# Performance work log

Measured on AMD Instinct MI355X. Metric: run time of the kernel, lower is better.

The kernel has to match this reference:

```python
import jax, jax.numpy as jnp
import numpy as np
import math

N_NODES, CHANNELS, N_ELEM, N_FEAT = 4096, 128, 10, 128
LS_IN = [0, 1, 2]          # input irreps per channel: 0e+1o+2e -> dim 9
L_OUT = [0, 1]             # keep_irrep_out = {0e, 1o}
L12_MAX = 3                # cap on intermediate coupling
SLICES = {0: (0, 1), 1: (1, 4), 2: (4, 9)}
PATHS1 = [l for l in L_OUT if l in LS_IN]
PATHS2 = [(l1, l2, lo) for l1 in LS_IN for l2 in LS_IN for lo in L_OUT if abs(l1 - l2) <= lo <= l1 + l2]
T12_KEYS = [(l1, l2, l12) for l1 in LS_IN for l2 in LS_IN for l12 in range(abs(l1 - l2), min(l1 + l2, L12_MAX) + 1)]
PATHS3 = [(k, l3, lo) for k in T12_KEYS for l3 in LS_IN for lo in L_OUT if abs(k[2] - l3) <= lo <= k[2] + l3]

def _su2_cg(j1, m1, j2, m2, j3, m3):
    if m3 != m1 + m2:
        return 0.0
    f = math.factorial
    vmin = max(-j1 + j2 + m3, -j1 + m1, 0)
    vmax = min(j2 + j3 + m1, j3 - j1 + j2, j3 + m3)
    C = math.sqrt((2 * j3 + 1) * f(j3 + j1 - j2) * f(j3 - j1 + j2) * f(j1 + j2 - j3) * f(j3 + m3) * f(j3 - m3)
                  / (f(j1 + j2 + j3 + 1) * f(j1 - m1) * f(j1 + m1) * f(j2 - m2) * f(j2 + m2)))
    S = 0.0
    for v in range(vmin, vmax + 1):
        S += (-1) ** (v + j2 + m2) * f(j2 + j3 + m1 - v) * f(j1 - m1 + v) / (
            f(v) * f(j3 - j1 + j2 - v) * f(j3 + m3 - v) * f(v + j1 - j2 - m3))
    return C * S

def _c2r(l):
    # change of basis real -> complex spherical harmonics (e3nn convention)
    q = np.zeros((2 * l + 1, 2 * l + 1), dtype=np.complex128)
    for m in range(-l, 0):
        q[l + m, l + abs(m)] = 1.0 / math.sqrt(2)
        q[l + m, l - abs(m)] = -1j / math.sqrt(2)
    q[l, l] = 1.0
    for m in range(1, l + 1):
        q[l + m, l + abs(m)] = (-1) ** m / math.sqrt(2)
        q[l + m, l - abs(m)] = 1j * (-1) ** m / math.sqrt(2)
    return (-1j) ** l * q

_CG = {}
def real_cg(l1, l2, l3):
    key = (l1, l2, l3)
    if key not in _CG:
        Cc = np.zeros((2 * l1 + 1, 2 * l2 + 1, 2 * l3 + 1), dtype=np.complex128)
        for i, m1 in enumerate(range(-l1, l1 + 1)):
            for j, m2 in enumerate(range(-l2, l2 + 1)):
                for k, m3 in enumerate(range(-l3, l3 + 1)):
                    Cc[i, j, k] = _su2_cg(l1, m1, l2, m2, l3, m3)
        R = np.einsum('ij,kl,mn,ikn->jlm', _c2r(l1), _c2r(l2), np.conj(_c2r(l3).T), Cc)
        _CG[key] = np.real(R).astype(np.float32)
    return _CG[key]

def setup_inputs():
    key = jax.random.key(0)
    k = jax.random.split(key, 8)
    node_feats = jax.random.normal(k[0], (N_NODES, CHANNELS, 9), dtype=jnp.float32)
    species = jax.random.randint(k[1], (N_NODES,), 0, N_ELEM)
    w1 = jax.random.normal(k[2], (N_ELEM, len(PATHS1), CHANNELS), dtype=jnp.float32) / math.sqrt(len(PATHS1))
    w2 = jax.random.normal(k[3], (N_ELEM, len(PATHS2), CHANNELS), dtype=jnp.float32) / math.sqrt(len(PATHS2))
    w3 = jax.random.normal(k[4], (N_ELEM, len(PATHS3), CHANNELS), dtype=jnp.float32) / math.sqrt(len(PATHS3))
    lin_w0 = jax.random.normal(k[5], (CHANNELS, N_FEAT), dtype=jnp.float32)
    lin_w1 = jax.random.normal(k[6], (CHANNELS, N_FEAT), dtype=jnp.float32)
    return {"node_feats": node_feats, "w1": w1, "w2": w2, "w3": w3,
            "lin_w0": lin_w0, "lin_w1": lin_w1, "species": species}

def reference(node_feats, w1, w2, w3, lin_w0, lin_w1, species):
    n, c = node_feats.shape[:2]
    attrs = jax.nn.one_hot(species, N_ELEM, dtype=node_feats.dtype)
    A = {l: node_feats[..., SLICES[l][0]:SLICES[l][1]] for l in LS_IN}
    # element-dependent path weights per node
    w1n = jnp.einsum('ne,epc->npc', attrs, w1)
    w2n = jnp.einsum('ne,epc->npc', attrs, w2)
    w3n = jnp.einsum('ne,epc->npc', attrs, w3)
    B = {lo: jnp.zeros((n, c, 2 * lo + 1), node_feats.dtype) for lo in L_OUT}
    # correlation order 1
    for p, lo in enumerate(PATHS1):
        B[lo] = B[lo] + w1n[:, p, :, None] * A[lo]
    for p, (l1, l2, lo) in enumerate(PATHS2):
        cg = jnp.asarray(real_cg(l1, l2, lo))
        t = jnp.einsum('ijk,nci,ncj->nck', cg, A[l1], A[l2])
        B[lo] = B[lo] + w2n[:, p, :, None] * t
    T12 = {}
    for kk in T12_KEYS:
        l1, l2, l12 = kk
        T12[kk] = jnp.einsum('ijk,nci,ncj->nck', jnp.asarray(real_cg(l1, l2, l12)), A[l1], A[l2])
    for p, (kk, l3, lo) in enumerate(PATHS3):
        cg = jnp.asarray(real_cg(kk[2], l3, lo))
        t = jnp.einsum('ijk,nci,ncj->nck', cg, T12[kk], A[l3])
        B[lo] = B[lo] + w3n[:, p, :, None] * t
    # equivariant Linear: mix channel axis into num_features per output irrep
    s = 1.0 / math.sqrt(c)
    out0 = jnp.einsum('ncm,cf->nfm', B[0], lin_w0) * s
    out1 = jnp.einsum('ncm,cf->nfm', B[1], lin_w1) * s
    return jnp.concatenate([out0, out1], axis=-1)  # [N, F, 1+3]
```

## Files before the change

### kernel.cpp

```cpp
#include <hip/hip_runtime.h>
#include <utility>


#define NN 4096
#define NC 128
#define NE 10

typedef float v2f __attribute__((ext_vector_type(2)));
typedef __bf16 bf16x8 __attribute__((ext_vector_type(8)));
typedef float f32x4 __attribute__((ext_vector_type(4)));

__device__ __forceinline__ v2f ld2(const float* p) {
  return *reinterpret_cast<const v2f*>(p);
}
__device__ __forceinline__ v2f cfma(float c, v2f x, v2f a) {
  v2f cc = {c, c};
  return __builtin_elementwise_fma(cc, x, a);
}
__device__ __forceinline__ v2f vfma(v2f w, v2f x, v2f a) {
  return __builtin_elementwise_fma(w, x, a);
}

__device__ __forceinline__ unsigned short f2bf(float x) {
  unsigned int u = __float_as_uint(x);
  unsigned int r = (u + 0x7FFFu + ((u >> 16) & 1u)) >> 16;
  return (unsigned short)r;
}
__device__ __forceinline__ float bf2f(unsigned short h) {
  return __uint_as_float(((unsigned int)h) << 16);
}

template<typename F, int... Is>
__device__ __forceinline__ void sfor_impl(F&& f, std::integer_sequence<int, Is...>) {
  (f(std::integral_constant<int, Is>{}), ...);
}
template<int N, typename F>
__device__ __forceinline__ void sfor(F&& f) {
  sfor_impl((F&&)f, std::make_integer_sequence<int, N>{});
}

constexpr int T_L1c[19]  = {0,0,0,1,1,1,1,1,1,1,2,2,2,2,2,2,2,2,3};
constexpr int T_L2c[19]  = {0,1,2,0,1,1,1,2,2,2,0,1,1,1,2,2,2,2,2};
constexpr int T_L3c[19]  = {0,1,2,1,0,1,2,1,2,3,2,1,2,3,0,1,2,3,1};
constexpr int T_OFFc[19] = {0,1,10,35,44,53,80,125,170,245,350,375,420,495,600,625,700,825,1000};
constexpr int AOFFc[3]   = {0,1,4};

constexpr int P2U_L1c[7]  = {0,0,1,1,1,2,2};
constexpr int P2U_L2c[7]  = {0,1,1,1,2,2,2};
constexpr int P2U_LOc[7]  = {0,1,0,1,1,0,1};
constexpr int P2U_TBLc[7] = {0,1,4,5,7,14,15};
constexpr int P2U_WAc[7]  = {0,1,3,4,5,7,8};
constexpr int P2U_WBc[7]  = {-1,2,-1,-1,6,-1,-1};

constexpr int K_L1c[18]  = {0,0,0,1,1,1,1,1,1,1,2,2,2,2,2,2,2,2};
constexpr int K_L2c[18]  = {0,1,2,0,1,1,1,2,2,2,0,1,1,1,2,2,2,2};
constexpr int K_L12c[18] = {0,1,2,1,0,1,2,1,2,3,2,1,2,3,0,1,2,3};

constexpr int   TT_CANONc[18] = {0,1,2,1,4,5,6,7,8,9,2,7,8,9,14,15,16,17};
constexpr float TT_SGNc[18]   = {1,1,1,1,1,1,1,1,1,1,1,1,-1,1,1,1,1,1};
constexpr int CANONc[13] = {0,1,2,4,5,6,7,8,9,14,15,16,17};
constexpr int CONS2c[13] = {-1,3,10,-1,-1,-1,11,12,13,-1,-1,-1,-1};

constexpr int P3_STARTc[19] = {0,2,6,9,13,15,19,22,26,29,30,33,37,40,41,43,47,50,51};
constexpr int P3_L3c[51] = {
  0,1,  0,1,1,2,  1,2,2,  0,1,1,2,  0,1,  0,1,1,2,  1,2,2,  0,1,1,2,  1,2,2,
  2,  1,2,2,  0,1,1,2,  1,2,2,  2,  0,1,  0,1,1,2,  1,2,2,  2 };
constexpr int P3_LOc[51] = {
  0,1,  1,0,1,1,  1,0,1,  1,0,1,1,  0,1,  1,0,1,1,  1,0,1,  1,0,1,1,  1,0,1,
  1,  1,0,1,  1,0,1,1,  1,0,1,  1,  0,1,  1,0,1,1,  1,0,1,  1 };
constexpr int P3_TBLc[51] = {
  0,1,  3,4,5,7,  11,14,15,  3,4,5,7,  0,1,  3,4,5,7,  11,14,15,  3,4,5,7,
  11,14,15,  18,  11,14,15,  3,4,5,7,  11,14,15,  18,  0,1,  3,4,5,7,
  11,14,15,  18 };

constexpr double cfact(int n) { double r = 1.0; for (int i = 2; i <= n; ++i) r *= i; return r; }
constexpr double csqrt(double x) {
  if (x <= 0.0) return 0.0;
  double r = x > 1.0 ? x : 1.0;
  for (int i = 0; i < 64; ++i) r = 0.5 * (r + x / r);
  return r;
}
constexpr double su2cg(int j1, int m1, int j2, int m2, int j3, int m3) {
  if (m3 != m1 + m2) return 0.0;
  int vmin = -j1 + j2 + m3; if (-j1 + m1 > vmin) vmin = -j1 + m1; if (vmin < 0) vmin = 0;
  int vmax = j2 + j3 + m1; if (j3 - j1 + j2 < vmax) vmax = j3 - j1 + j2; if (j3 + m3 < vmax) vmax = j3 + m3;
  double C = csqrt((2.0 * j3 + 1.0)
                   * cfact(j3 + j1 - j2) * cfact(j3 - j1 + j2) * cfact(j1 + j2 - j3)
                   * cfact(j3 + m3) * cfact(j3 - m3)
                   / (cfact(j1 + j2 + j3 + 1) * cfact(j1 - m1) * cfact(j1 + m1)
                      * cfact(j2 - m2) * cfact(j2 + m2)));
  double S = 0.0;
  for (int v = vmin; v <= vmax; ++v) {
    double sgn = ((v + j2 + m2) & 1) ? -1.0 : 1.0;
    S += sgn * cfact(j2 + j3 + m1 - v) * cfact(j1 - m1 + v)
         / (cfact(v) * cfact(j3 - j1 + j2 - v) * cfact(j3 + m3 - v) * cfact(v + j1 - j2 - m3));
  }
  return C * S;
}

struct Cx { double re, im; };
constexpr Cx cxmul(Cx a, Cx b) { return Cx{a.re * b.re - a.im * b.im, a.re * b.im + a.im * b.re}; }
struct Row { int cnt; int col[2]; Cx v[2]; };

constexpr Row c2r_row(int l, int r) {
  Row out{0, {0, 0}, {{0, 0}, {0, 0}}};
  constexpr double is2 = 0.70710678118654752440;
  const int m = r - l;
  if (m < 0) {
    out.cnt = 2;
    out.col[0] = l - m; out.v[0] = Cx{is2, 0.0};
    out.col[1] = l + m; out.v[1] = Cx{0.0, -is2};
  } else if (m == 0) {
    out.cnt = 1; out.col[0] = l; out.v[0] = Cx{1.0, 0.0};
  } else {
    const double sgn = (m & 1) ? -1.0 : 1.0;
    out.cnt = 2;
    out.col[0] = l + m; out.v[0] = Cx{sgn * is2, 0.0};
    out.col[1] = l - m; out.v[1] = Cx{0.0, sgn * is2};
  }
  const int ph = l & 3;
  for (int a = 0; a < out.cnt; ++a) {
    Cx v = out.v[a];
    out.v[a] = (ph == 0) ? v
             : (ph == 1) ? Cx{v.im, -v.re}
             : (ph == 2) ? Cx{-v.re, -v.im}
                         : Cx{-v.im, v.re};
  }
  return out;
}

struct CGAll { float v[1105]; };
constexpr CGAll make_cg() {
  CGAll R{};
  for (int t = 0; t < 19; ++t) {
    const int l1 = T_L1c[t], l2 = T_L2c[t], l3 = T_L3c[t], off = T_OFFc[t];
    const int d1 = 2 * l1 + 1, d2 = 2 * l2 + 1, d3 = 2 * l3 + 1;
    double tmp[175] = {};
    for (int i = 0; i < d1; ++i) {
      const int m1 = i - l1;
      const Row r1 = c2r_row(l1, i);
      for (int k = 0; k < d2; ++k) {
        const int m2 = k - l2, m3 = m1 + m2;
        if (m3 < -l3 || m3 > l3) continue;
        const double cc = su2cg(l1, m1, l2, m2, l3, m3);
        if (cc == 0.0) continue;
        const Row r2 = c2r_row(l2, k);
        const Row r3 = c2r_row(l3, m3 + l3);
        for (int a = 0; a < r1.cnt; ++a)
          for (int b = 0; b < r2.cnt; ++b) {
            const Cx q12 = cxmul(r1.v[a], r2.v[b]);
            for (int cdx = 0; cdx < r3.cnt; ++cdx) {
              const double re = q12.re * r3.v[cdx].re + q12.im * r3.v[cdx].im;
              tmp[(r1.col[a] * d2 + r2.col[b]) * d3 + r3.col[cdx]] += re * cc;
            }
          }
      }
    }
    const int sz = d1 * d2 * d3;
    for (int e = 0; e < sz; ++e) R.v[off + e] = (float)tmp[e];
  }
  return R;
}
constexpr CGAll CG_ALL = make_cg();

constexpr bool check_cg_sym() {
  for (int t = 0; t < 18; ++t) {
    const int tc = TT_CANONc[t];
    if (tc == t) continue;
    const int l1 = K_L1c[t], l2 = K_L2c[t], l12 = K_L12c[t];
    const int d1 = 2*l1+1, d2 = 2*l2+1, d12 = 2*l12+1;
    for (int i = 0; i < d1; ++i)
      for (int j = 0; j < d2; ++j)
        for (int k = 0; k < d12; ++k) {
          float a = CG_ALL.v[T_OFFc[t]  + (i*d2 + j)*d12 + k];
          float b = TT_SGNc[t] * CG_ALL.v[T_OFFc[tc] + (j*d1 + i)*d12 + k];
          float d = a - b; if (d < 0) d = -d;
          if (d > 1e-5f) return false;
        }
  }
  return true;
}
static_assert(check_cg_sym(), "CG exchange symmetry violated");

__global__ __launch_bounds__(256) void epb_basis(
    const float* __restrict__ nf,
    const float* __restrict__ w1,
    const float* __restrict__ w2,
    const float* __restrict__ w3,
    const int*   __restrict__ species,
    unsigned int* __restrict__ AhiW,
    unsigned int* __restrict__ AloW)
{
  const int t  = threadIdx.x;
  const int nb = blockIdx.x * 4;
  const int nl = t >> 6;
  const int c0 = (t & 63) * 2;
  const int n  = nb + nl;
  const int s  = species[n];

  const float* ap = nf + ((size_t)n * NC + c0) * 9;
  v2f A[9];
  sfor<9>([&](auto I) { A[I.value] = v2f{ap[I.value], ap[I.value + 9]}; });

  const float* w1p = w1 + (size_t)s * 2  * NC + c0;
  const float* w2p = w2 + (size_t)s * 9  * NC + c0;
  const float* w3p = w3 + (size_t)s * 51 * NC + c0;

  v2f B[4];
  {
    const v2f wa = ld2(w1p), wb = ld2(w1p + NC);
    B[0] = wa * A[0];
    B[1] = wb * A[1];
    B[2] = wb * A[2];
    B[3] = wb * A[3];
  }

  sfor<7>([&](auto P) {
    constexpr int p  = P.value;
    constexpr int l1 = P2U_L1c[p], l2 = P2U_L2c[p], lo = P2U_LOc[p];
    constexpr int d1 = 2*l1+1, d2 = 2*l2+1, dl = 2*lo+1;
    constexpr int off = T_OFFc[P2U_TBLc[p]];
    v2f w = ld2(w2p + P2U_WAc[p] * NC);
    if constexpr (P2U_WBc[p] >= 0) w = w + ld2(w2p + P2U_WBc[p] * NC);
    sfor<dl>([&](auto Kk) {
      constexpr int k = Kk.value;
      v2f v = {0.f, 0.f};
      sfor<d1>([&](auto I) {
        sfor<d2>([&](auto J) {
          constexpr float cgc = CG_ALL.v[off + (I.value * d2 + J.value) * dl + k];
          if constexpr (cgc != 0.0f) {
            constexpr int ia = AOFFc[l1] + I.value, ja = AOFFc[l2] + J.value;
            constexpr int x = ia < ja ? ia : ja, y = ia < ja ? ja : ia;
            v = cfma(cgc, A[x] * A[y], v);
          }
        });
      });
      B[lo + k] = vfma(w, v, B[lo + k]);
    });
  });

  sfor<13>([&](auto CI) {
    constexpr int tk  = CANONc[CI.value];
    constexpr int l1  = K_L1c[tk], l2 = K_L2c[tk], l12 = K_L12c[tk];
    constexpr int d1  = 2*l1+1, d2 = 2*l2+1, d12 = 2*l12+1;
    constexpr int off = T_OFFc[tk];
    v2f tt[d12];
    sfor<d12>([&](auto Kk) {
      constexpr int k = Kk.value;
      v2f v = {0.f, 0.f};
      sfor<d1>([&](auto I) {
        sfor<d2>([&](auto J) {
          constexpr float cgc = CG_ALL.v[off + (I.value * d2 + J.value) * d12 + k];
          if constexpr (cgc != 0.0f) {
            constexpr int ia = AOFFc[l1] + I.value, ja = AOFFc[l2] + J.value;
            constexpr int x = ia < ja ? ia : ja, y = ia < ja ? ja : ia;
            v = cfma(cgc, A[x] * A[y], v);
          }
        });
      });
      tt[k] = v;
    });

    auto consume = [&](auto TK, auto SG) {
      constexpr int tkey = TK.value;
      constexpr float sgn = (float)SG.value;
      constexpr int pcnt = P3_STARTc[tkey + 1] - P3_STARTc[tkey];
      sfor<pcnt>([&](auto PP) {
        constexpr int p  = P3_STARTc[tkey] + PP.value;
        constexpr int l3 = P3_L3c[p], lo = P3_LOc[p];
        constexpr int d3 = 2*l3+1, dl = 2*lo+1;
        constexpr int off2 = T_OFFc[P3_TBLc[p]];
        const v2f w = ld2(w3p + p * NC);
        sfor<dl>([&](auto M) {
          v2f v = {0.f, 0.f};
          sfor<d12>([&](auto Kk) {
            sfor<d3>([&](auto J) {
              constexpr float cgc = sgn * CG_ALL.v[off2 + (Kk.value * d3 + J.value) * dl + M.value];
              if constexpr (cgc != 0.0f)
                v = cfma(cgc, tt[Kk.value] * A[AOFFc[l3] + J.value], v);
            });
          });
          B[lo + M.value] = vfma(w, v, B[lo + M.value]);
        });
      });
    };
    consume(std::integral_constant<int, tk>{}, std::integral_constant<int, 1>{});
    constexpr int td = CONS2c[CI.value];
    if constexpr (td >= 0)
      consume(std::integral_constant<int, td>{},
              std::integral_constant<int, (int)TT_SGNc[td]>{});
  });

  const int idx = n * 64 + (c0 >> 1);
  sfor<4>([&](auto M) {
    constexpr int m = M.value;
    const float x0 = B[m].x, x1 = B[m].y;
    const unsigned short h0 = f2bf(x0), h1 = f2bf(x1);
    const unsigned short l0 = f2bf(x0 - bf2f(h0)), l1 = f2bf(x1 - bf2f(h1));
    AhiW[m * (NN * 64) + idx] = ((unsigned int)h1 << 16) | h0;
    AloW[m * (NN * 64) + idx] = ((unsigned int)l1 << 16) | l0;
  });
}

__global__ __launch_bounds__(256) void wt_pack(
    const float* __restrict__ lw0, const float* __restrict__ lw1,
    unsigned short* __restrict__ Wt)
{
  const int tid = blockIdx.x * 256 + threadIdx.x;
  const int mat = tid >> 14;
  const int rr  = tid & 16383;
  const int f   = rr >> 7, c = rr & 127;
  const float x = (mat ? lw1 : lw0)[c * NC + f];
  const unsigned short h = f2bf(x);
  const unsigned short l = f2bf(x - bf2f(h));
  unsigned short* base = Wt + mat * 2 * (NC * NC);
  base[f * NC + c]           = h;
  base[NC * NC + f * NC + c] = l;
}

__global__ __launch_bounds__(256) void epb_linear_mfma(
    const unsigned short* __restrict__ Ahi,
    const unsigned short* __restrict__ Alo,
    const unsigned short* __restrict__ Wt,
    float* __restrict__ out)
{
  const int lane = threadIdx.x & 63;
  const int T = blockIdx.x * 4 + (threadIdx.x >> 6);
  const int m  = T >> 11;
  const int r  = T & 2047;
  const int n0 = (r >> 3) * 16;
  const int f0 = (r & 7) * 16;

  const unsigned short* Whi = Wt + (m == 0 ? 0 : 2) * (NC * NC);
  const unsigned short* Wlo = Whi + NC * NC;

  const int row  = lane & 15;
  const int quad = lane >> 4;

  const unsigned short* ah = Ahi + (size_t)m * (NN * NC) + (n0 + row) * NC + quad * 8;
  const unsigned short* al = Alo + (size_t)m * (NN * NC) + (n0 + row) * NC + quad * 8;
  const unsigned short* wh = Whi + (f0 + row) * NC + quad * 8;
  const unsigned short* wl = Wlo + (f0 + row) * NC + quad * 8;

  f32x4 acc = {0.f, 0.f, 0.f, 0.f};
  sfor<4>([&](auto KC) {
    constexpr int c0 = KC.value * 32;
    const bf16x8 a_h = *reinterpret_cast<const bf16x8*>(ah + c0);
    const bf16x8 a_l = *reinterpret_cast<const bf16x8*>(al + c0);
    const bf16x8 w_h = *reinterpret_cast<const bf16x8*>(wh + c0);
    const bf16x8 w_l = *reinterpret_cast<const bf16x8*>(wl + c0);
    acc = __builtin_amdgcn_mfma_f32_16x16x32_bf16(a_h, w_h, acc, 0, 0, 0);
    acc = __builtin_amdgcn_mfma_f32_16x16x32_bf16(a_h, w_l, acc, 0, 0, 0);
    acc = __builtin_amdgcn_mfma_f32_16x16x32_bf16(a_l, w_h, acc, 0, 0, 0);
    acc = __builtin_amdgcn_mfma_f32_16x16x32_bf16(a_l, w_l, acc, 0, 0, 0);
  });

  const float s4 = 0.08838834764831845f;
  const int f = f0 + row;
  const int nbase = n0 + quad * 4;
  sfor<4>([&](auto R) {
    out[(size_t)(nbase + R.value) * 512 + f * 4 + m] = acc[R.value] * s4;
  });
}

extern "C" void kernel_launch(void* const* d_in, const int* in_sizes, int n_in,
                              void* d_out, int out_size, void* d_ws, size_t ws_size,
                              hipStream_t stream) {
  const float* nf  = (const float*)d_in[0];
  const float* w1  = (const float*)d_in[1];
  const float* w2  = (const float*)d_in[2];
  const float* w3  = (const float*)d_in[3];
  const float* lw0 = (const float*)d_in[4];
  const float* lw1 = (const float*)d_in[5];
  const int*   spc = (const int*)  d_in[6];
  float* out = (float*)d_out;

  unsigned short* Ahi = (unsigned short*)d_ws;
  unsigned short* Alo = Ahi + (size_t)4 * NN * NC;
  unsigned short* Wt  = Alo + (size_t)4 * NN * NC;
  (void)ws_size; (void)in_sizes; (void)n_in; (void)out_size;

  hipLaunchKernelGGL(wt_pack, dim3(32768 / 256), dim3(256), 0, stream,
                     lw0, lw1, Wt);
  hipLaunchKernelGGL(epb_basis, dim3(NN / 4), dim3(256), 0, stream,
                     nf, w1, w2, w3, spc, (unsigned int*)Ahi, (unsigned int*)Alo);
  hipLaunchKernelGGL(epb_linear_mfma, dim3(8192 / 4), dim3(256), 0, stream,
                     Ahi, Alo, Wt, out);
}
```

Baseline: 107.3 us.

## Fuse basis computation and MFMA linear into one kernel via shared memory

The symmetric-contraction basis kernel and the MFMA channel-mixing kernel become a single kernel. Each 512-thread block computes B for 8 nodes, stores the bf16 hi/lo split in LDS, and then runs the 16x16x32 MFMA tiles directly from LDS. This removes the global-memory round trip of the intermediate hi/lo A buffers and one kernel launch. In exchange, half of each 16-row MFMA tile is wasted because only 8 nodes exist per block (those rows are discarded), the grid has fewer and larger blocks, and each block re-reads the weight matrices from cache.

After: 105.8 us. About the same (-1.5%).

```diff
diff --git a/kernel.cpp b/kernel.cpp
--- a/kernel.cpp
+++ b/kernel.cpp
@@ -182,126 +182,6 @@
 }
 static_assert(check_cg_sym(), "CG exchange symmetry violated");
 
-__global__ __launch_bounds__(256) void epb_basis(
-    const float* __restrict__ nf,
-    const float* __restrict__ w1,
-    const float* __restrict__ w2,
-    const float* __restrict__ w3,
-    const int*   __restrict__ species,
-    unsigned int* __restrict__ AhiW,
-    unsigned int* __restrict__ AloW)
-{
-  const int t  = threadIdx.x;
-  const int nb = blockIdx.x * 4;
-  const int nl = t >> 6;
-  const int c0 = (t & 63) * 2;
-  const int n  = nb + nl;
-  const int s  = species[n];
-
-  const float* ap = nf + ((size_t)n * NC + c0) * 9;
-  v2f A[9];
-  sfor<9>([&](auto I) { A[I.value] = v2f{ap[I.value], ap[I.value + 9]}; });
-
-  const float* w1p = w1 + (size_t)s * 2  * NC + c0;
-  const float* w2p = w2 + (size_t)s * 9  * NC + c0;
-  const float* w3p = w3 + (size_t)s * 51 * NC + c0;
-
-  v2f B[4];
-  {
-    const v2f wa = ld2(w1p), wb = ld2(w1p + NC);
-    B[0] = wa * A[0];
-    B[1] = wb * A[1];
-    B[2] = wb * A[2];
-    B[3] = wb * A[3];
-  }
-
-  sfor<7>([&](auto P) {
-    constexpr int p  = P.value;
-    constexpr int l1 = P2U_L1c[p], l2 = P2U_L2c[p], lo = P2U_LOc[p];
-    constexpr int d1 = 2*l1+1, d2 = 2*l2+1, dl = 2*lo+1;
-    constexpr int off = T_OFFc[P2U_TBLc[p]];
-    v2f w = ld2(w2p + P2U_WAc[p] * NC);
-    if constexpr (P2U_WBc[p] >= 0) w = w + ld2(w2p + P2U_WBc[p] * NC);
-    sfor<dl>([&](auto Kk) {
-      constexpr int k = Kk.value;
-      v2f v = {0.f, 0.f};
-      sfor<d1>([&](auto I) {
-        sfor<d2>([&](auto J) {
-          constexpr float cgc = CG_ALL.v[off + (I.value * d2 + J.value) * dl + k];
-          if constexpr (cgc != 0.0f) {
-            constexpr int ia = AOFFc[l1] + I.value, ja = AOFFc[l2] + J.value;
-            constexpr int x = ia < ja ? ia : ja, y = ia < ja ? ja : ia;
-            v = cfma(cgc, A[x] * A[y], v);
-          }
-        });
-      });
-      B[lo + k] = vfma(w, v, B[lo + k]);
-    });
-  });
-
-  sfor<13>([&](auto CI) {
-    constexpr int tk  = CANONc[CI.value];
-    constexpr int l1  = K_L1c[tk], l2 = K_L2c[tk], l12 = K_L12c[tk];
-    constexpr int d1  = 2*l1+1, d2 = 2*l2+1, d12 = 2*l12+1;
-    constexpr int off = T_OFFc[tk];
-    v2f tt[d12];
-    sfor<d12>([&](auto Kk) {
-      constexpr int k = Kk.value;
-      v2f v = {0.f, 0.f};
-      sfor<d1>([&](auto I) {
-        sfor<d2>([&](auto J) {
-          constexpr float cgc = CG_ALL.v[off + (I.value * d2 + J.value) * d12 + k];
-          if constexpr (cgc != 0.0f) {
-            constexpr int ia = AOFFc[l1] + I.value, ja = AOFFc[l2] + J.value;
-            constexpr int x = ia < ja ? ia : ja, y = ia < ja ? ja : ia;
-            v = cfma(cgc, A[x] * A[y], v);
-          }
-        });
-      });
-      tt[k] = v;
-    });
-
-    auto consume = [&](auto TK, auto SG) {
-      constexpr int tkey = TK.value;
-      constexpr float sgn = (float)SG.value;
-      constexpr int pcnt = P3_STARTc[tkey + 1] - P3_STARTc[tkey];
-      sfor<pcnt>([&](auto PP) {
-        constexpr int p  = P3_STARTc[tkey] + PP.value;
-        constexpr int l3 = P3_L3c[p], lo = P3_LOc[p];
-        constexpr int d3 = 2*l3+1, dl = 2*lo+1;
-        constexpr int off2 = T_OFFc[P3_TBLc[p]];
-        const v2f w = ld2(w3p + p * NC);
-        sfor<dl>([&](auto M) {
-          v2f v = {0.f, 0.f};
-          sfor<d12>([&](auto Kk) {
-            sfor<d3>([&](auto J) {
-              constexpr float cgc = sgn * CG_ALL.v[off2 + (Kk.value * d3 + J.value) * dl + M.value];
-              if constexpr (cgc != 0.0f)
-                v = cfma(cgc, tt[Kk.value] * A[AOFFc[l3] + J.value], v);
-            });
-          });
-          B[lo + M.value] = vfma(w, v, B[lo + M.value]);
-        });
-      });
-    };
-    consume(std::integral_constant<int, tk>{}, std::integral_constant<int, 1>{});
-    constexpr int td = CONS2c[CI.value];
-    if constexpr (td >= 0)
-      consume(std::integral_constant<int, td>{},
-              std::integral_constant<int, (int)TT_SGNc[td]>{});
-  });
-
-  const int idx = n * 64 + (c0 >> 1);
-  sfor<4>([&](auto M) {
-    constexpr int m = M.value;
-    const float x0 = B[m].x, x1 = B[m].y;
-    const unsigned short h0 = f2bf(x0), h1 = f2bf(x1);
-    const unsigned short l0 = f2bf(x0 - bf2f(h0)), l1 = f2bf(x1 - bf2f(h1));
-    AhiW[m * (NN * 64) + idx] = ((unsigned int)h1 << 16) | h0;
-    AloW[m * (NN * 64) + idx] = ((unsigned int)l1 << 16) | l0;
-  });
-}
-
 __global__ __launch_bounds__(256) void wt_pack(
     const float* __restrict__ lw0, const float* __restrict__ lw1,
     unsigned short* __restrict__ Wt)
@@ -318,48 +198,168 @@
   base[NC * NC + f * NC + c] = l;
 }
 
-__global__ __launch_bounds__(256) void epb_linear_mfma(
-    const unsigned short* __restrict__ Ahi,
-    const unsigned short* __restrict__ Alo,
+#define MATS 2176
+__global__ __launch_bounds__(512) void epb_fused(
+    const float* __restrict__ nf,
+    const float* __restrict__ w1,
+    const float* __restrict__ w2,
+    const float* __restrict__ w3,
+    const int*   __restrict__ species,
     const unsigned short* __restrict__ Wt,
     float* __restrict__ out)
 {
-  const int lane = threadIdx.x & 63;
-  const int T = blockIdx.x * 4 + (threadIdx.x >> 6);
-  const int m  = T >> 11;
-  const int r  = T & 2047;
-  const int n0 = (r >> 3) * 16;
-  const int f0 = (r & 7) * 16;
-
-  const unsigned short* Whi = Wt + (m == 0 ? 0 : 2) * (NC * NC);
-  const unsigned short* Wlo = Whi + NC * NC;
+  __shared__ unsigned short Ash[8 * MATS];
+  const int t    = threadIdx.x;
+  const int nb   = blockIdx.x * 8;
+  const int wave = t >> 6, lane = t & 63;
+
+  {
+    const int nl = wave, c0 = lane * 2;
+    const int n  = nb + nl;
+    const int s  = species[n];
+
+    const float* ap = nf + ((size_t)n * NC + c0) * 9;
+    v2f A[9];
+    sfor<9>([&](auto I) { A[I.value] = v2f{ap[I.value], ap[I.value + 9]}; });
+
+    const float* w1p = w1 + (size_t)s * 2  * NC + c0;
+    const float* w2p = w2 + (size_t)s * 9  * NC + c0;
+    const float* w3p = w3 + (size_t)s * 51 * NC + c0;
+
+    v2f B[4];
+    {
+      const v2f wa = ld2(w1p), wb = ld2(w1p + NC);
+      B[0] = wa * A[0];
+      B[1] = wb * A[1];
+      B[2] = wb * A[2];
+      B[3] = wb * A[3];
+    }
+
+    sfor<7>([&](auto P) {
+      constexpr int p  = P.value;
+      constexpr int l1 = P2U_L1c[p], l2 = P2U_L2c[p], lo = P2U_LOc[p];
+      constexpr int d1 = 2*l1+1, d2 = 2*l2+1, dl = 2*lo+1;
+      constexpr int off = T_OFFc[P2U_TBLc[p]];
+      v2f w = ld2(w2p + P2U_WAc[p] * NC);
+      if constexpr (P2U_WBc[p] >= 0) w = w + ld2(w2p + P2U_WBc[p] * NC);
+      sfor<dl>([&](auto Kk) {
+        constexpr int k = Kk.value;
+        v2f v = {0.f, 0.f};
+        sfor<d1>([&](auto I) {
+          sfor<d2>([&](auto J) {
+            constexpr float cgc = CG_ALL.v[off + (I.value * d2 + J.value) * dl + k];
+            if constexpr (cgc != 0.0f) {
+              constexpr int ia = AOFFc[l1] + I.value, ja = AOFFc[l2] + J.value;
+              constexpr int x = ia < ja ? ia : ja, y = ia < ja ? ja : ia;
+              v = cfma(cgc, A[x] * A[y], v);
+            }
+          });
+        });
+        B[lo + k] = vfma(w, v, B[lo + k]);
+      });
+    });
+
+    sfor<13>([&](auto CI) {
+      constexpr int tk  = CANONc[CI.value];
+      constexpr int l1  = K_L1c[tk], l2 = K_L2c[tk], l12 = K_L12c[tk];
+      constexpr int d1  = 2*l1+1, d2 = 2*l2+1, d12 = 2*l12+1;
+      constexpr int off = T_OFFc[tk];
+      v2f tt[d12];
+      sfor<d12>([&](auto Kk) {
+        constexpr int k = Kk.value;
+        v2f v = {0.f, 0.f};
+        sfor<d1>([&](auto I) {
+          sfor<d2>([&](auto J) {
+            constexpr float cgc = CG_ALL.v[off + (I.value * d2 + J.value) * d12 + k];
+            if constexpr (cgc != 0.0f) {
+              constexpr int ia = AOFFc[l1] + I.value, ja = AOFFc[l2] + J.value;
+              constexpr int x = ia < ja ? ia : ja, y = ia < ja ? ja : ia;
+              v = cfma(cgc, A[x] * A[y], v);
+            }
+          });
+        });
+        tt[k] = v;
+      });
+
+      auto consume = [&](auto TK, auto SG) {
+        constexpr int tkey = TK.value;
+        constexpr float sgn = (float)SG.value;
+        constexpr int pcnt = P3_STARTc[tkey + 1] - P3_STARTc[tkey];
+        sfor<pcnt>([&](auto PP) {
+          constexpr int p  = P3_STARTc[tkey] + PP.value;
+          constexpr int l3 = P3_L3c[p], lo = P3_LOc[p];
+          constexpr int d3 = 2*l3+1, dl = 2*lo+1;
+          constexpr int off2 = T_OFFc[P3_TBLc[p]];
+          const v2f w = ld2(w3p + p * NC);
+          sfor<dl>([&](auto M) {
+            v2f v = {0.f, 0.f};
+            sfor<d12>([&](auto Kk) {
+              sfor<d3>([&](auto J) {
+                constexpr float cgc = sgn * CG_ALL.v[off2 + (Kk.value * d3 + J.value) * dl + M.value];
+                if constexpr (cgc != 0.0f)
+                  v = cfma(cgc, tt[Kk.value] * A[AOFFc[l3] + J.value], v);
+              });
+            });
+            B[lo + M.value] = vfma(w, v, B[lo + M.value]);
+          });
+        });
+      };
+      consume(std::integral_constant<int, tk>{}, std::integral_constant<int, 1>{});
+      constexpr int td = CONS2c[CI.value];
+      if constexpr (td >= 0)
+        consume(std::integral_constant<int, td>{},
+                std::integral_constant<int, (int)TT_SGNc[td]>{});
+    });
+
+    unsigned int* Au = reinterpret_cast<unsigned int*>(Ash);
+    sfor<4>([&](auto M) {
+      constexpr int m = M.value;
+      const float x0 = B[m].x, x1 = B[m].y;
+      const unsigned short h0 = f2bf(x0), h1 = f2bf(x1);
+      const unsigned short l0 = f2bf(x0 - bf2f(h0)), l1 = f2bf(x1 - bf2f(h1));
+      Au[(2*m)     * (MATS/2) + nl * 68 + lane] = ((unsigned int)h1 << 16) | h0;
+      Au[(2*m + 1) * (MATS/2) + nl * 68 + lane] = ((unsigned int)l1 << 16) | l0;
+    });
+  }
+  __syncthreads();
 
   const int row  = lane & 15;
   const int quad = lane >> 4;
-
-  const unsigned short* ah = Ahi + (size_t)m * (NN * NC) + (n0 + row) * NC + quad * 8;
-  const unsigned short* al = Alo + (size_t)m * (NN * NC) + (n0 + row) * NC + quad * 8;
-  const unsigned short* wh = Whi + (f0 + row) * NC + quad * 8;
-  const unsigned short* wl = Wlo + (f0 + row) * NC + quad * 8;
-
-  f32x4 acc = {0.f, 0.f, 0.f, 0.f};
-  sfor<4>([&](auto KC) {
-    constexpr int c0 = KC.value * 32;
-    const bf16x8 a_h = *reinterpret_cast<const bf16x8*>(ah + c0);
-    const bf16x8 a_l = *reinterpret_cast<const bf16x8*>(al + c0);
-    const bf16x8 w_h = *reinterpret_cast<const bf16x8*>(wh + c0);
-    const bf16x8 w_l = *reinterpret_cast<const bf16x8*>(wl + c0);
-    acc = __builtin_amdgcn_mfma_f32_16x16x32_bf16(a_h, w_h, acc, 0, 0, 0);
-    acc = __builtin_amdgcn_mfma_f32_16x16x32_bf16(a_h, w_l, acc, 0, 0, 0);
-    acc = __builtin_amdgcn_mfma_f32_16x16x32_bf16(a_l, w_h, acc, 0, 0, 0);
-    acc = __builtin_amdgcn_mfma_f32_16x16x32_bf16(a_l, w_l, acc, 0, 0, 0);
-  });
-
   const float s4 = 0.08838834764831845f;
-  const int f = f0 + row;
-  const int nbase = n0 + quad * 4;
-  sfor<4>([&](auto R) {
-    out[(size_t)(nbase + R.value) * 512 + f * 4 + m] = acc[R.value] * s4;
+
+  sfor<4>([&](auto TI) {
+    const int tile = wave * 4 + TI.value;
+    const int m    = tile >> 3;
+    const int f0   = (tile & 7) * 16;
+
+    const unsigned short* Whi = Wt + (m == 0 ? 0 : 2) * (NC * NC);
+    const unsigned short* Wlo = Whi + NC * NC;
+    const unsigned short* wh = Whi + (f0 + row) * NC + quad * 8;
+    const unsigned short* wl = Wlo + (f0 + row) * NC + quad * 8;
+
+    const unsigned short* ah = Ash + (2*m)     * MATS + row * 136 + quad * 8;
+    const unsigned short* al = Ash + (2*m + 1) * MATS + row * 136 + quad * 8;
+
+    f32x4 acc = {0.f, 0.f, 0.f, 0.f};
+    sfor<4>([&](auto KC) {
+      constexpr int c0 = KC.value * 32;
+      const bf16x8 a_h = *reinterpret_cast<const bf16x8*>(ah + c0);
+      const bf16x8 a_l = *reinterpret_cast<const bf16x8*>(al + c0);
+      const bf16x8 w_h = *reinterpret_cast<const bf16x8*>(wh + c0);
+      const bf16x8 w_l = *reinterpret_cast<const bf16x8*>(wl + c0);
+      acc = __builtin_amdgcn_mfma_f32_16x16x32_bf16(a_h, w_h, acc, 0, 0, 0);
+      acc = __builtin_amdgcn_mfma_f32_16x16x32_bf16(a_h, w_l, acc, 0, 0, 0);
+      acc = __builtin_amdgcn_mfma_f32_16x16x32_bf16(a_l, w_h, acc, 0, 0, 0);
+      acc = __builtin_amdgcn_mfma_f32_16x16x32_bf16(a_l, w_l, acc, 0, 0, 0);
+    });
+
+    if (quad < 2) {
+      const int f = f0 + row;
+      sfor<4>([&](auto R) {
+        const int nl2 = quad * 4 + R.value;
+        out[(size_t)(nb + nl2) * 512 + f * 4 + m] = acc[R.value] * s4;
+      });
+    }
   });
 }
 
@@ -374,16 +374,11 @@
   const float* lw1 = (const float*)d_in[5];
   const int*   spc = (const int*)  d_in[6];
   float* out = (float*)d_out;
-
-  unsigned short* Ahi = (unsigned short*)d_ws;
-  unsigned short* Alo = Ahi + (size_t)4 * NN * NC;
-  unsigned short* Wt  = Alo + (size_t)4 * NN * NC;
+  unsigned short* Wt = (unsigned short*)d_ws;
   (void)ws_size; (void)in_sizes; (void)n_in; (void)out_size;
 
   hipLaunchKernelGGL(wt_pack, dim3(32768 / 256), dim3(256), 0, stream,
                      lw0, lw1, Wt);
-  hipLaunchKernelGGL(epb_basis, dim3(NN / 4), dim3(256), 0, stream,
-                     nf, w1, w2, w3, spc, (unsigned int*)Ahi, (unsigned int*)Alo);
-  hipLaunchKernelGGL(epb_linear_mfma, dim3(8192 / 4), dim3(256), 0, stream,
-                     Ahi, Alo, Wt, out);
-}
+  hipLaunchKernelGGL(epb_fused, dim3(NN / 8), dim3(512), 0, stream,
+                     nf, w1, w2, w3, spc, Wt, out);
+}
```
